# Kernel tuning notes

Hardware: AMD Instinct MI355X
Metric: run time of the kernel (lower is better)

## Reference

```python
import jax, jax.numpy as jnp
import numpy as np

TEMPERATURE = 0.5
EPS = 1e-8  # torch CosineSimilarity default eps


def setup_inputs() -> dict:
    key = jax.random.key(0)
    k1, k2 = jax.random.split(key)
    N, D = 4096, 256
    return {
        "batch_embeddings": jax.random.normal(k1, (N, D), dtype=jnp.float32),
        "batch_augmented_embeddings": jax.random.normal(k2, (N, D), dtype=jnp.float32),
    }


def reference(batch_embeddings, batch_augmented_embeddings):
    N = batch_embeddings.shape[0]
    emb = jnp.concatenate([batch_embeddings, batch_augmented_embeddings], axis=0)  # (2N, D)
    # cosine similarity = normalized dot products (normalize + GEMM rewrite of the
    # broadcasted nn.CosineSimilarity)
    norms = jnp.sqrt(jnp.sum(emb * emb, axis=-1, keepdims=True))
    emb_n = emb / jnp.maximum(norms, EPS)
    sim = jnp.einsum("id,jd->ij", emb_n, emb_n) / TEMPERATURE  # (2N, 2N)
    # negative mask: (~eye(N)).repeat(2,2) -> False where (i mod N) == (j mod N)
    idx = jnp.arange(2 * N)
    neg_mask = (idx[:, None] % N) != (idx[None, :] % N)
    exp_sim = jnp.exp(sim) * neg_mask.astype(sim.dtype)
    sum_exp = jnp.sum(exp_sim, axis=-1)  # (2N,)
    pos = jnp.arange(N)
    positive_sim = sim[pos, N + pos]  # (N,)
    negative_sim_sum = sum_exp[:N]  # (N,)
    loss = -jnp.mean(jnp.log(jnp.exp(positive_sim) / negative_sim_sum))
    return loss
```

## Files before the change

### kernel.cpp

```cpp
#include <hip/hip_runtime.h>
#include <hip/hip_bf16.h>

#define NROWS 4096
#define DDIM  256
#define EPS   1e-8f
#define SCALE 1.69864944f
#define LN2   0.69314718056f

#define NJ 32
#define JS 256
#define BT 64
#define CH (JS / BT)
#define BUFSH (4 * 8 * 64 * 8)

typedef __attribute__((ext_vector_type(8))) short short8;
typedef __attribute__((ext_vector_type(4))) float f32x4;

#if __has_builtin(__builtin_amdgcn_exp2f)
#define EXP2F(x) __builtin_amdgcn_exp2f(x)
#else
#define EXP2F(x) exp2f(x)
#endif

__device__ __forceinline__ unsigned short f2bf(float x) {
    union { __hip_bfloat16 h; unsigned short u; } c;
    c.h = __float2bfloat16(x);
    return c.u;
}

__device__ __forceinline__ float bf2f(unsigned short u) {
    union { float f; unsigned int i; } c;
    c.i = ((unsigned int)u) << 16;
    return c.f;
}

__global__ void prep_kernel(const float* __restrict__ a,
                            const float* __restrict__ b,
                            unsigned short* __restrict__ en,
                            float* __restrict__ S,
                            float* __restrict__ pos, int N) {
    const int wave = threadIdx.x >> 6, lane = threadIdx.x & 63;
    const int row = blockIdx.x * 4 + wave;
    const float4 va = reinterpret_cast<const float4*>(a + (size_t)row * DDIM)[lane];
    const float4 vb = reinterpret_cast<const float4*>(b + (size_t)row * DDIM)[lane];
    float ssa = va.x * va.x + va.y * va.y + va.z * va.z + va.w * va.w;
    float ssb = vb.x * vb.x + vb.y * vb.y + vb.z * vb.z + vb.w * vb.w;
    #pragma unroll
    for (int off = 32; off > 0; off >>= 1) {
        ssa += __shfl_xor(ssa, off);
        ssb += __shfl_xor(ssb, off);
    }
    const float inva = SCALE / fmaxf(sqrtf(ssa), EPS * SCALE);
    const float invb = SCALE / fmaxf(sqrtf(ssb), EPS * SCALE);
    ushort4 oa, ob;
    oa.x = f2bf(va.x * inva); oa.y = f2bf(va.y * inva);
    oa.z = f2bf(va.z * inva); oa.w = f2bf(va.w * inva);
    ob.x = f2bf(vb.x * invb); ob.y = f2bf(vb.y * invb);
    ob.z = f2bf(vb.z * invb); ob.w = f2bf(vb.w * invb);
    *reinterpret_cast<ushort4*>(en + (size_t)row * DDIM + lane * 4) = oa;
    *reinterpret_cast<ushort4*>(en + (size_t)(N + row) * DDIM + lane * 4) = ob;
    float d = bf2f(oa.x) * bf2f(ob.x) + bf2f(oa.y) * bf2f(ob.y) +
              bf2f(oa.z) * bf2f(ob.z) + bf2f(oa.w) * bf2f(ob.w);
    #pragma unroll
    for (int off = 32; off > 0; off >>= 1) d += __shfl_xor(d, off);
    if (lane == 0) {
        pos[row] = d * LN2;
        S[row] = 0.0f;
    }
}

__global__ __launch_bounds__(512, 2) void simsum_kernel(
        const short* __restrict__ en,
        float* __restrict__ S) {
    __shared__ short bt[2 * BUFSH];
    const int tid = threadIdx.x;
    const int wave = tid >> 6, lane = tid & 63;
    const int lrow = lane & 15, quad = lane >> 4;
    const int i0 = blockIdx.x * 256 + wave * 32;
    const int jb = blockIdx.y * JS;

    short8 afrag[2][8];
    #pragma unroll
    for (int t = 0; t < 2; ++t)
        #pragma unroll
        for (int ks = 0; ks < 8; ++ks)
            afrag[t][ks] = *reinterpret_cast<const short8*>(
                en + (size_t)(i0 + t * 16 + lrow) * DDIM + ks * 32 + quad * 8);

    float rowsum[2][4];
    #pragma unroll
    for (int t = 0; t < 2; ++t)
        #pragma unroll
        for (int r = 0; r < 4; ++r) rowsum[t][r] = 0.0f;

    const int scg = wave >> 1, skh = (wave & 1) * 4;
    auto stage = [&](int jc, int buf) {
        const short* g = en + (size_t)(jc + scg * 16 + lrow) * DDIM
                         + skh * 32 + quad * 8;
        short* l = bt + buf * BUFSH + scg * 4096 + skh * 512;
        #pragma unroll
        for (int ks = 0; ks < 4; ++ks) {
            __builtin_amdgcn_global_load_lds(
                (const __attribute__((address_space(1))) void*)(g + ks * 32),
                (__attribute__((address_space(3))) void*)(l + ks * 512),
                16, 0, 0);
        }
    };

    stage(jb, 0);
    for (int c = 0; c < CH; ++c) {
        asm volatile("s_waitcnt lgkmcnt(0)" ::: "memory");
        __builtin_amdgcn_s_barrier();
        if (c + 1 < CH) {
            stage(jb + (c + 1) * BT, (c + 1) & 1);
            asm volatile("s_waitcnt vmcnt(4)" ::: "memory");
        } else {
            asm volatile("s_waitcnt vmcnt(0)" ::: "memory");
        }
        __builtin_amdgcn_sched_barrier(0);
        __builtin_amdgcn_s_barrier();
        const short* lb = bt + (c & 1) * BUFSH;
        #pragma unroll
        for (int cg = 0; cg < 4; ++cg) {
            f32x4 acc[2];
            #pragma unroll
            for (int t = 0; t < 2; ++t) acc[t] = f32x4{0.f, 0.f, 0.f, 0.f};
            __builtin_amdgcn_s_setprio(1);
            #pragma unroll
            for (int ks = 0; ks < 8; ++ks) {
                const short8 bfrag = *reinterpret_cast<const short8*>(
                    lb + cg * 4096 + ks * 512 + lane * 8);
                #pragma unroll
                for (int t = 0; t < 2; ++t)
                    acc[t] = __builtin_amdgcn_mfma_f32_16x16x32_bf16(
                        afrag[t][ks], bfrag, acc[t], 0, 0, 0);
            }
            __builtin_amdgcn_s_setprio(0);
            const int cm = (jb + c * BT + cg * 16 + lrow) & (NROWS - 1);
            #pragma unroll
            for (int t = 0; t < 2; ++t) {
                const int dd = cm - (i0 + t * 16 + quad * 4);
                #pragma unroll
                for (int r = 0; r < 4; ++r) {
                    const float ed = EXP2F(acc[t][r]);
                    rowsum[t][r] += (dd == r) ? 0.0f : ed;
                }
            }
        }
    }

    #pragma unroll
    for (int t = 0; t < 2; ++t) {
        #pragma unroll
        for (int r = 0; r < 4; ++r) {
            float v = rowsum[t][r];
            v += __shfl_xor(v, 1);
            v += __shfl_xor(v, 2);
            v += __shfl_xor(v, 4);
            v += __shfl_xor(v, 8);
            rowsum[t][r] = v;
        }
        if (lrow < 4) {
            const float v = (lrow == 0) ? rowsum[t][0]
                          : (lrow == 1) ? rowsum[t][1]
                          : (lrow == 2) ? rowsum[t][2]
                          :               rowsum[t][3];
            atomicAdd(&S[i0 + t * 16 + quad * 4 + lrow], v);
        }
    }
}

__global__ void loss_kernel(const float* __restrict__ S,
                            const float* __restrict__ pos,
                            float* __restrict__ out, int N) {
    const int i = threadIdx.x * 4;
    float acc = 0.0f;
    if (i < N) {
        const float4 s4 = *reinterpret_cast<const float4*>(S + i);
        const float4 p4 = *reinterpret_cast<const float4*>(pos + i);
        acc = (p4.x - __logf(s4.x)) + (p4.y - __logf(s4.y)) +
              (p4.z - __logf(s4.z)) + (p4.w - __logf(s4.w));
    }
    #pragma unroll
    for (int off = 32; off > 0; off >>= 1) acc += __shfl_xor(acc, off);
    __shared__ float wsum[16];
    const int wave = threadIdx.x >> 6, lane = threadIdx.x & 63;
    if (lane == 0) wsum[wave] = acc;
    __syncthreads();
    if (threadIdx.x == 0) {
        float tot = 0.0f;
        #pragma unroll
        for (int w = 0; w < 16; ++w) tot += wsum[w];
        out[0] = -tot / (float)N;
    }
}

extern "C" void kernel_launch(void* const* d_in, const int* in_sizes, int n_in,
                              void* d_out, int out_size, void* d_ws, size_t ws_size,
                              hipStream_t stream) {
    const float* a = (const float*)d_in[0];
    const float* b = (const float*)d_in[1];
    float* out = (float*)d_out;
    const int N = NROWS;

    char* ws = (char*)d_ws;
    unsigned short* en = (unsigned short*)ws;
    float* S = (float*)(ws + (size_t)2 * N * DDIM * sizeof(unsigned short));
    float* pos = S + N;

    prep_kernel<<<N / 4, 256, 0, stream>>>(a, b, en, S, pos, N);
    simsum_kernel<<<dim3(NROWS / 256, NJ), 512, 0, stream>>>((const short*)en, S);
    loss_kernel<<<1, 1024, 0, stream>>>(S, pos, out, N);
}
```

Measured before the change: 90.87 us.

## Use 4-wave blocks with 64-row tiles and ping-pong MFMA/exp epilogue

Halves the block to 256 threads so each wave now owns 64 rows (4 A-fragment tiles) instead of 32, doubling B-fragment reuse per LDS read. Each wave now stages a full 16-column group of the B tile. The inner loop alternates two accumulator sets so the exp/masked-sum epilogue of one column group is interleaved with the MFMAs of the next, hiding transcendental latency. This raises register pressure (twice the A fragments and two accumulator sets) and halves the number of waves per block, which may reduce occupancy and latency hiding.

```diff
diff --git a/kernel.cpp b/kernel.cpp
--- a/kernel.cpp
+++ b/kernel.cpp
@@ -69,37 +69,35 @@
     }
 }
 
-__global__ __launch_bounds__(512, 2) void simsum_kernel(
+__global__ __launch_bounds__(256, 2) void simsum_kernel(
         const short* __restrict__ en,
         float* __restrict__ S) {
     __shared__ short bt[2 * BUFSH];
     const int tid = threadIdx.x;
     const int wave = tid >> 6, lane = tid & 63;
     const int lrow = lane & 15, quad = lane >> 4;
-    const int i0 = blockIdx.x * 256 + wave * 32;
+    const int i0 = blockIdx.x * 256 + wave * 64;
     const int jb = blockIdx.y * JS;
 
-    short8 afrag[2][8];
-    #pragma unroll
-    for (int t = 0; t < 2; ++t)
+    short8 afrag[4][8];
+    #pragma unroll
+    for (int t = 0; t < 4; ++t)
         #pragma unroll
         for (int ks = 0; ks < 8; ++ks)
             afrag[t][ks] = *reinterpret_cast<const short8*>(
                 en + (size_t)(i0 + t * 16 + lrow) * DDIM + ks * 32 + quad * 8);
 
-    float rowsum[2][4];
-    #pragma unroll
-    for (int t = 0; t < 2; ++t)
+    float rowsum[4][4];
+    #pragma unroll
+    for (int t = 0; t < 4; ++t)
         #pragma unroll
         for (int r = 0; r < 4; ++r) rowsum[t][r] = 0.0f;
 
-    const int scg = wave >> 1, skh = (wave & 1) * 4;
     auto stage = [&](int jc, int buf) {
-        const short* g = en + (size_t)(jc + scg * 16 + lrow) * DDIM
-                         + skh * 32 + quad * 8;
-        short* l = bt + buf * BUFSH + scg * 4096 + skh * 512;
-        #pragma unroll
-        for (int ks = 0; ks < 4; ++ks) {
+        const short* g = en + (size_t)(jc + wave * 16 + lrow) * DDIM + quad * 8;
+        short* l = bt + buf * BUFSH + wave * 4096;
+        #pragma unroll
+        for (int ks = 0; ks < 8; ++ks) {
             __builtin_amdgcn_global_load_lds(
                 (const __attribute__((address_space(1))) void*)(g + ks * 32),
                 (__attribute__((address_space(3))) void*)(l + ks * 512),
@@ -107,13 +105,44 @@
         }
     };
 
+#define MFMA_TILE(ACC, LB, CG) do {                                          \
+        _Pragma("unroll")                                                    \
+        for (int t = 0; t < 4; ++t) ACC[t] = f32x4{0.f, 0.f, 0.f, 0.f};      \
+        _Pragma("unroll")                                                    \
+        for (int ks = 0; ks < 8; ++ks) {                                     \
+            const short8 bfrag = *reinterpret_cast<const short8*>(           \
+                (LB) + (CG) * 4096 + ks * 512 + lane * 8);                   \
+            _Pragma("unroll")                                                \
+            for (int t = 0; t < 4; ++t)                                      \
+                ACC[t] = __builtin_amdgcn_mfma_f32_16x16x32_bf16(            \
+                    afrag[t][ks], bfrag, ACC[t], 0, 0, 0);                   \
+        }                                                                    \
+    } while (0)
+
+#define EPI_TILE(ACC, COL) do {                                              \
+        const int cm_ = (COL) & (NROWS - 1);                                 \
+        _Pragma("unroll")                                                    \
+        for (int t = 0; t < 4; ++t) {                                        \
+            const int dd_ = cm_ - (i0 + t * 16 + quad * 4);                  \
+            _Pragma("unroll")                                                \
+            for (int r = 0; r < 4; ++r) {                                    \
+                const float ed_ = EXP2F(ACC[t][r]);                          \
+                rowsum[t][r] += (dd_ == r) ? 0.0f : ed_;                     \
+            }                                                                \
+        }                                                                    \
+    } while (0)
+
+    f32x4 acc0[4], acc1[4];
+    int pcol = 0;
+
     stage(jb, 0);
+    #pragma unroll
     for (int c = 0; c < CH; ++c) {
         asm volatile("s_waitcnt lgkmcnt(0)" ::: "memory");
         __builtin_amdgcn_s_barrier();
         if (c + 1 < CH) {
             stage(jb + (c + 1) * BT, (c + 1) & 1);
-            asm volatile("s_waitcnt vmcnt(4)" ::: "memory");
+            asm volatile("s_waitcnt vmcnt(8)" ::: "memory");
         } else {
             asm volatile("s_waitcnt vmcnt(0)" ::: "memory");
         }
@@ -121,36 +150,21 @@
         __builtin_amdgcn_s_barrier();
         const short* lb = bt + (c & 1) * BUFSH;
         #pragma unroll
-        for (int cg = 0; cg < 4; ++cg) {
-            f32x4 acc[2];
-            #pragma unroll
-            for (int t = 0; t < 2; ++t) acc[t] = f32x4{0.f, 0.f, 0.f, 0.f};
-            __builtin_amdgcn_s_setprio(1);
-            #pragma unroll
-            for (int ks = 0; ks < 8; ++ks) {
-                const short8 bfrag = *reinterpret_cast<const short8*>(
-                    lb + cg * 4096 + ks * 512 + lane * 8);
-                #pragma unroll
-                for (int t = 0; t < 2; ++t)
-                    acc[t] = __builtin_amdgcn_mfma_f32_16x16x32_bf16(
-                        afrag[t][ks], bfrag, acc[t], 0, 0, 0);
-            }
-            __builtin_amdgcn_s_setprio(0);
-            const int cm = (jb + c * BT + cg * 16 + lrow) & (NROWS - 1);
-            #pragma unroll
-            for (int t = 0; t < 2; ++t) {
-                const int dd = cm - (i0 + t * 16 + quad * 4);
-                #pragma unroll
-                for (int r = 0; r < 4; ++r) {
-                    const float ed = EXP2F(acc[t][r]);
-                    rowsum[t][r] += (dd == r) ? 0.0f : ed;
-                }
-            }
-        }
-    }
-
-    #pragma unroll
-    for (int t = 0; t < 2; ++t) {
+        for (int cg = 0; cg < 4; cg += 2) {
+            MFMA_TILE(acc0, lb, cg);
+            if (c > 0 || cg > 0) EPI_TILE(acc1, pcol);
+            pcol = jb + c * BT + cg * 16 + lrow;
+            MFMA_TILE(acc1, lb, cg + 1);
+            EPI_TILE(acc0, pcol);
+            pcol = jb + c * BT + (cg + 1) * 16 + lrow;
+        }
+    }
+    EPI_TILE(acc1, pcol);
+#undef MFMA_TILE
+#undef EPI_TILE
+
+    #pragma unroll
+    for (int t = 0; t < 4; ++t) {
         #pragma unroll
         for (int r = 0; r < 4; ++r) {
             float v = rowsum[t][r];
@@ -209,6 +223,6 @@
     float* pos = S + N;
 
     prep_kernel<<<N / 4, 256, 0, stream>>>(a, b, en, S, pos, N);
-    simsum_kernel<<<dim3(NROWS / 256, NJ), 512, 0, stream>>>((const short*)en, S);
+    simsum_kernel<<<dim3(NROWS / 256, NJ), 256, 0, stream>>>((const short*)en, S);
     loss_kernel<<<1, 1024, 0, stream>>>(S, pos, out, N);
 }
```

After: 96.83 us. +6.6%, slower.
